# Kernel tuning notes

Hardware: AMD Instinct MI355X
Metric: run time of the kernel (lower is better)

## Reference

```python
import jax, jax.numpy as jnp
import numpy as np

B, S, H, F, E, N, K = 2, 4096, 1024, 3584, 8, 2, 2


def setup_inputs() -> dict:
    key = jax.random.key(0)
    ks = jax.random.split(key, 6)
    scale_h = 1.0 / np.sqrt(H)
    scale_f = 1.0 / np.sqrt(F)
    return {
        "hidden_states": jax.random.normal(ks[0], (B, S, H), dtype=jnp.float32),
        "gate_w": jax.random.normal(ks[1], (E, H), dtype=jnp.float32) * scale_h,
        "gate2_w": jax.random.normal(ks[2], (N, H), dtype=jnp.float32) * scale_h,
        "w1": jax.random.normal(ks[3], (E, F, H), dtype=jnp.float32) * scale_h,
        "w2": jax.random.normal(ks[4], (E, H, F), dtype=jnp.float32) * scale_f,
        "w3": jax.random.normal(ks[5], (E, F, H), dtype=jnp.float32) * scale_h,
    }


def reference(hidden_states, gate_w, gate2_w, w1, w2, w3):
    b, s, h = hidden_states.shape
    x = hidden_states.reshape(-1, h)  # [T, H]

    # Router: real gate + null-expert gate, concatenated
    router_logits = jnp.concatenate([x @ gate_w.T, x @ gate2_w.T], axis=1)  # [T, E+N]
    rw = jax.nn.softmax(router_logits.astype(jnp.float32), axis=1)
    top_w, sel = jax.lax.top_k(rw, K)  # [T, K]

    # Null experts (idx >= E) get their raw weight; real experts are renormalized
    mask = sel < E
    sw = top_w * mask
    denom = sw.sum(axis=-1, keepdims=True)
    denom = jnp.where(denom == 0, 1.0, denom)
    weights = (sw / denom + top_w * (~mask)).astype(x.dtype)  # [T, K]

    # Per-(token, real-expert) combine weight; null experts drop out (one_hot -> 0)
    combine = jnp.einsum("tke,tk->et", jax.nn.one_hot(sel, E, dtype=x.dtype), weights)  # [E, T]

    def body(acc, p):
        w1e, w2e, w3e, cw = p
        hgate = jax.nn.silu(x @ w1e.T) * (x @ w3e.T)  # [T, F]
        return acc + cw[:, None] * (hgate @ w2e.T), None

    out, _ = jax.lax.scan(body, jnp.zeros_like(x), (w1, w2, w3, combine))
    return out.reshape(b, s, h), router_logits
```

## Files before the change

kernel.cpp:

```cpp
#include <hip/hip_runtime.h>
#include <hip/hip_bf16.h>

namespace {

constexpr int T_TOK = 8192;
constexpr int HDIM  = 1024;
constexpr int FDIM  = 3584;
constexpr int CAP_ROWS = 18432;
constexpr int MAXMT = CAP_ROWS / 256;

typedef __bf16 bf16x8 __attribute__((ext_vector_type(8)));
typedef float  f32x4  __attribute__((ext_vector_type(4)));

__device__ inline unsigned short f2bf(float f) {
  union { float f; unsigned u; } a; a.f = f;
  unsigned r = a.u + 0x7fffu + ((a.u >> 16) & 1u);
  return (unsigned short)(r >> 16);
}

typedef const __attribute__((address_space(1))) void* gptr_t;
typedef __attribute__((address_space(3))) void* lptr_t;
__device__ inline void gload_lds16(const void* g, void* l) {
  __builtin_amdgcn_global_load_lds((gptr_t)g, (lptr_t)l, 16, 0, 0);
}

#define MFMA16(a, b, c) __builtin_amdgcn_mfma_f32_16x16x32_bf16(a, b, c, 0, 0, 0)

__global__ __launch_bounds__(256) void k_router(
    const float* __restrict__ x, const float* __restrict__ gw,
    const float* __restrict__ gw2, float* __restrict__ logits_out,
    int* __restrict__ sel, float* __restrict__ wts)
{
  int t = blockIdx.x * 4 + (threadIdx.x >> 6);
  int lane = threadIdx.x & 63;
  if (t >= T_TOK) return;
  const float* xr = x + (size_t)t * HDIM;
  float acc[10];
#pragma unroll
  for (int e = 0; e < 10; ++e) acc[e] = 0.f;
#pragma unroll
  for (int it = 0; it < 4; ++it) {
    int base = it * 256 + lane * 4;
    float4 xv = *reinterpret_cast<const float4*>(xr + base);
#pragma unroll
    for (int e = 0; e < 8; ++e) {
      float4 g = *reinterpret_cast<const float4*>(gw + e * HDIM + base);
      acc[e] += xv.x * g.x + xv.y * g.y + xv.z * g.z + xv.w * g.w;
    }
#pragma unroll
    for (int e = 0; e < 2; ++e) {
      float4 g = *reinterpret_cast<const float4*>(gw2 + e * HDIM + base);
      acc[8 + e] += xv.x * g.x + xv.y * g.y + xv.z * g.z + xv.w * g.w;
    }
  }
#pragma unroll
  for (int e = 0; e < 10; ++e) {
#pragma unroll
    for (int off = 32; off > 0; off >>= 1)
      acc[e] += __shfl_xor(acc[e], off, 64);
  }
  if (lane == 0) {
    float* lo = logits_out + (size_t)t * 10;
#pragma unroll
    for (int e = 0; e < 10; ++e) lo[e] = acc[e];
    float mx = acc[0];
#pragma unroll
    for (int e = 1; e < 10; ++e) mx = fmaxf(mx, acc[e]);
    float p[10], s = 0.f;
#pragma unroll
    for (int e = 0; e < 10; ++e) { p[e] = __expf(acc[e] - mx); s += p[e]; }
    float inv = 1.f / s;
#pragma unroll
    for (int e = 0; e < 10; ++e) p[e] *= inv;
    int i0 = 0;
    for (int e = 1; e < 10; ++e) if (p[e] > p[i0]) i0 = e;
    int i1 = (i0 == 0) ? 1 : 0;
    for (int e = 0; e < 10; ++e) if (e != i0 && p[e] > p[i1]) i1 = e;
    float w0 = p[i0], w1 = p[i1];
    bool r0 = i0 < 8, r1 = i1 < 8;
    float den = (r0 ? w0 : 0.f) + (r1 ? w1 : 0.f);
    if (den == 0.f) den = 1.f;
    sel[t * 2]     = i0; wts[t * 2]     = r0 ? w0 / den : 0.f;
    sel[t * 2 + 1] = i1; wts[t * 2 + 1] = r1 ? w1 / den : 0.f;
  }
}

__global__ __launch_bounds__(256) void k_histseg(
    const int* __restrict__ sel, int* __restrict__ meta)
{
  __shared__ int part[256][8];
  __shared__ int s_tile0[9];
  int tid = threadIdx.x;
  int c[8];
#pragma unroll
  for (int e = 0; e < 8; ++e) c[e] = 0;
  for (int i = 0; i < 64; ++i) {
    int v = sel[i * 256 + tid];
#pragma unroll
    for (int e = 0; e < 8; ++e) c[e] += (v == e);
  }
#pragma unroll
  for (int e = 0; e < 8; ++e) part[tid][e] = c[e];
  __syncthreads();
  for (int s = 128; s >= 1; s >>= 1) {
    if (tid < s) {
#pragma unroll
      for (int e = 0; e < 8; ++e) part[tid][e] += part[tid + s][e];
    }
    __syncthreads();
  }
  if (tid == 0) {
    int off = 0;
    for (int e = 0; e < 8; ++e) {
      int cnt = part[0][e];
      meta[e] = cnt;
      meta[8 + e] = 0;
      meta[16 + e] = off;
      s_tile0[e] = off >> 8;
      off += (cnt + 255) & ~255;
    }
    meta[24] = off;
    meta[25] = off >> 8;
    s_tile0[8] = off >> 8;
  }
  __syncthreads();
  int nt = s_tile0[8];
  if (tid < nt) {
    int e = 0;
    while (s_tile0[e + 1] <= tid) ++e;
    meta[32 + tid] = e;
  }
}

__global__ __launch_bounds__(256) void k_zeropad(
    const int* __restrict__ meta, unsigned short* __restrict__ xg)
{
  int e = blockIdx.x >> 8, r = blockIdx.x & 255;
  int c = meta[e];
  int pad = (c + 255) & ~255;
  if (c + r >= pad) return;
  size_t row = (size_t)meta[16 + e] + c + r;
  reinterpret_cast<ushort4*>(xg + row * HDIM)[threadIdx.x] = ushort4{0, 0, 0, 0};
}

__global__ __launch_bounds__(256) void k_scatter(
    const float* __restrict__ x, const int* __restrict__ sel,
    int* __restrict__ meta, int* __restrict__ pair_row,
    unsigned short* __restrict__ xg)
{
  __shared__ int s_cnt[8];
  __shared__ int s_base[8];
  __shared__ int s_row[256];
  int tid = threadIdx.x;
  int pair0 = blockIdx.x * 256;
  if (tid < 8) s_cnt[tid] = 0;
  __syncthreads();
  int e = sel[pair0 + tid];
  int rank = -1;
  if (e < 8) rank = atomicAdd(&s_cnt[e], 1);
  __syncthreads();
  if (tid < 8) {
    int c = s_cnt[tid];
    s_base[tid] = c > 0 ? atomicAdd(&meta[8 + tid], c) : 0;
  }
  __syncthreads();
  int row = (e < 8) ? meta[16 + e] + s_base[e] + rank : -1;
  pair_row[pair0 + tid] = row;
  s_row[tid] = row;
  __syncthreads();
  int wid = tid >> 6, lane = tid & 63;
  for (int i = wid; i < 256; i += 4) {
    int r = s_row[i];
    if (r < 0) continue;
    const float* xr = x + (size_t)((pair0 + i) >> 1) * HDIM;
    unsigned short* dst = xg + (size_t)r * HDIM;
#pragma unroll
    for (int it = 0; it < 4; ++it) {
      int base = it * 256 + lane * 4;
      float4 v = *reinterpret_cast<const float4*>(xr + base);
      ushort4 o{f2bf(v.x), f2bf(v.y), f2bf(v.z), f2bf(v.w)};
      *reinterpret_cast<ushort4*>(dst + base) = o;
    }
  }
}

__global__ __launch_bounds__(256) void k_conv3(
    const float* __restrict__ s1, const float* __restrict__ s3,
    const float* __restrict__ s2,
    unsigned short* __restrict__ d1, unsigned short* __restrict__ d3,
    unsigned short* __restrict__ d2,
    long long total, long long rl13, long long ss13,
    long long rl2, long long ss2)
{
  long long i = ((long long)blockIdx.x * 256 + threadIdx.x) * 8;
  if (i >= total) return;
  const float* src; unsigned short* dst; long long rowlen, sstride;
  if (blockIdx.y == 0)      { src = s1; dst = d1; rowlen = rl13; sstride = ss13; }
  else if (blockIdx.y == 1) { src = s3; dst = d3; rowlen = rl13; sstride = ss13; }
  else                      { src = s2; dst = d2; rowlen = rl2;  sstride = ss2;  }
  const float* sp;
  if (rowlen == sstride) {
    sp = src + i;
  } else {
    long long r = i / rowlen, c = i - r * rowlen;
    sp = src + r * sstride + c;
  }
  float4 a = reinterpret_cast<const float4*>(sp)[0];
  float4 b = reinterpret_cast<const float4*>(sp)[1];
  ushort4* d = reinterpret_cast<ushort4*>(dst + i);
  d[0] = ushort4{f2bf(a.x), f2bf(a.y), f2bf(a.z), f2bf(a.w)};
  d[1] = ushort4{f2bf(b.x), f2bf(b.y), f2bf(b.z), f2bf(b.w)};
}

__global__ __launch_bounds__(512, 2) void k_gemm1(
    const unsigned short* __restrict__ xg,
    const unsigned short* __restrict__ wc1,
    const unsigned short* __restrict__ wc3,
    unsigned short* __restrict__ hg,
    const int* __restrict__ meta, int Fc)
{
  __shared__ __attribute__((aligned(128))) char lds[131072];

  int mt = blockIdx.y;
  if (mt >= meta[25]) return;
  int e = meta[32 + mt];
  int mrow0 = mt * 256;
  int fl0 = blockIdx.x * 128;

  int tid = threadIdx.x, lane = tid & 63, wid = tid >> 6;
  int lr = lane & 15, lg = lane >> 4;
  int wr = wid >> 2, wc = wid & 3;

  f32x4 acc1[8][2], acc3[8][2];
  const f32x4 zero = {0.f, 0.f, 0.f, 0.f};
#pragma unroll
  for (int m = 0; m < 8; ++m)
#pragma unroll
    for (int n = 0; n < 2; ++n) { acc1[m][n] = zero; acc3[m][n] = zero; }

  int r0 = tid >> 3;
  int csw = ((tid & 7) ^ (r0 & 7)) * 8;
  int dst0 = tid * 16;

  const unsigned short* pa[4];
  const unsigned short* pb1[2];
  const unsigned short* pb3[2];
  {
    const unsigned short* Ab  = xg + (size_t)mrow0 * HDIM;
    const unsigned short* B1b = wc1 + ((size_t)e * Fc + fl0) * HDIM;
    const unsigned short* B3b = wc3 + ((size_t)e * Fc + fl0) * HDIM;
#pragma unroll
    for (int h = 0; h < 2; ++h)
#pragma unroll
      for (int q = 0; q < 2; ++q)
        pa[h * 2 + q] = Ab + (size_t)(h * 128 + q * 64 + r0) * HDIM + csw;
#pragma unroll
    for (int q = 0; q < 2; ++q) {
      pb1[q] = B1b + (size_t)(q * 64 + r0) * HDIM + csw;
      pb3[q] = B3b + (size_t)(q * 64 + r0) * HDIM + csw;
    }
  }

  auto STAGE = [&](int buf) {
    char* b = lds + buf * 65536;
#pragma unroll
    for (int i = 0; i < 4; ++i) {
      gload_lds16(pa[i], b + (i >> 1) * 16384 + (i & 1) * 8192 + dst0);
      pa[i] += 64;
    }
#pragma unroll
    for (int q = 0; q < 2; ++q) {
      gload_lds16(pb1[q], b + 32768 + q * 8192 + dst0);
      pb1[q] += 64;
      gload_lds16(pb3[q], b + 49152 + q * 8192 + dst0);
      pb3[q] += 64;
    }
  };

  const int fxor = (lr & 7) << 4;

  constexpr int NT = HDIM / 64;
  STAGE(0);
#pragma unroll 1
  for (int t = 0; t < NT; ++t) {
    int c = t & 1;
    if (t < NT - 1) {
      STAGE(c ^ 1);
      asm volatile("s_waitcnt vmcnt(8)" ::: "memory");
    } else {
      asm volatile("s_waitcnt vmcnt(0)" ::: "memory");
    }
    asm volatile("s_barrier" ::: "memory");

    const char* bb = lds + c * 65536;
    const char* ab = bb + wr * 16384;
#pragma unroll
    for (int kk = 0; kk < 2; ++kk) {
      int kbyte = (kk * 64 + lg * 16) ^ fxor;
      bf16x8 b1f[2], b3f[2];
#pragma unroll
      for (int n = 0; n < 2; ++n) {
        int off = (wc * 32 + n * 16 + lr) * 128 + kbyte;
        b1f[n] = *reinterpret_cast<const bf16x8*>(bb + 32768 + off);
        b3f[n] = *reinterpret_cast<const bf16x8*>(bb + 49152 + off);
      }
#pragma unroll
      for (int m = 0; m < 8; ++m) {
        bf16x8 af = *reinterpret_cast<const bf16x8*>(ab + (m * 16 + lr) * 128 + kbyte);
#pragma unroll
        for (int n = 0; n < 2; ++n) {
          acc1[m][n] = MFMA16(af, b1f[n], acc1[m][n]);
          acc3[m][n] = MFMA16(af, b3f[n], acc3[m][n]);
        }
      }
    }
    asm volatile("s_barrier" ::: "memory");
  }

#pragma unroll
  for (int m = 0; m < 8; ++m)
#pragma unroll
    for (int n = 0; n < 2; ++n) {
      int gcol = fl0 + wc * 32 + n * 16 + lr;
#pragma unroll
      for (int j = 0; j < 4; ++j) {
        int grow = mrow0 + wr * 128 + m * 16 + lg * 4 + j;
        float s1 = acc1[m][n][j];
        float s3 = acc3[m][n][j];
        float h = s1 / (1.f + __expf(-s1)) * s3;
        hg[(size_t)grow * Fc + gcol] = f2bf(h);
      }
    }
}

__global__ __launch_bounds__(512, 2) void k_gemm2(
    const unsigned short* __restrict__ hg,
    const unsigned short* __restrict__ wc2,
    float* __restrict__ yrows, const int* __restrict__ meta,
    int Fc, int first)
{
  __shared__ __attribute__((aligned(128))) char lds[98304];

  int mt = blockIdx.y;
  if (mt >= meta[25]) return;
  int e = meta[32 + mt];
  int mrow0 = mt * 256;
  int hcol0 = blockIdx.x * 128;

  int tid = threadIdx.x, lane = tid & 63, wid = tid >> 6;
  int lr = lane & 15, lg = lane >> 4;
  int wr = wid >> 2, wc = wid & 3;

  f32x4 acc[8][2];
  const f32x4 zero = {0.f, 0.f, 0.f, 0.f};
#pragma unroll
  for (int m = 0; m < 8; ++m)
#pragma unroll
    for (int n = 0; n < 2; ++n) acc[m][n] = zero;

  int r0 = tid >> 3;
  int csw = ((tid & 7) ^ (r0 & 7)) * 8;
  int dst0 = tid * 16;

  const unsigned short* pa[4];
  const unsigned short* pb[2];
  {
    const unsigned short* Ab = hg + (size_t)mrow0 * Fc;
    const unsigned short* Bb = wc2 + ((size_t)e * HDIM + hcol0) * Fc;
#pragma unroll
    for (int h = 0; h < 2; ++h)
#pragma unroll
      for (int q = 0; q < 2; ++q)
        pa[h * 2 + q] = Ab + (size_t)(h * 128 + q * 64 + r0) * Fc + csw;
#pragma unroll
    for (int q = 0; q < 2; ++q)
      pb[q] = Bb + (size_t)(q * 64 + r0) * Fc + csw;
  }

  auto STAGE = [&](int buf) {
    char* b = lds + buf * 49152;
#pragma unroll
    for (int i = 0; i < 4; ++i) {
      gload_lds16(pa[i], b + (i >> 1) * 16384 + (i & 1) * 8192 + dst0);
      pa[i] += 64;
    }
#pragma unroll
    for (int q = 0; q < 2; ++q) {
      gload_lds16(pb[q], b + 32768 + q * 8192 + dst0);
      pb[q] += 64;
    }
  };

  const int fxor = (lr & 7) << 4;

  int NT = Fc / 64;
  STAGE(0);
#pragma unroll 1
  for (int t = 0; t < NT; ++t) {
    int c = t & 1;
    if (t < NT - 1) {
      STAGE(c ^ 1);
      asm volatile("s_waitcnt vmcnt(6)" ::: "memory");
    } else {
      asm volatile("s_waitcnt vmcnt(0)" ::: "memory");
    }
    asm volatile("s_barrier" ::: "memory");

    const char* bb = lds + c * 49152;
    const char* ab = bb + wr * 16384;
#pragma unroll
    for (int kk = 0; kk < 2; ++kk) {
      int kbyte = (kk * 64 + lg * 16) ^ fxor;
      bf16x8 bf[2];
#pragma unroll
      for (int n = 0; n < 2; ++n) {
        int off = (wc * 32 + n * 16 + lr) * 128 + kbyte;
        bf[n] = *reinterpret_cast<const bf16x8*>(bb + 32768 + off);
      }
#pragma unroll
      for (int m = 0; m < 8; ++m) {
        bf16x8 af = *reinterpret_cast<const bf16x8*>(ab + (m * 16 + lr) * 128 + kbyte);
#pragma unroll
        for (int n = 0; n < 2; ++n)
          acc[m][n] = MFMA16(af, bf[n], acc[m][n]);
      }
    }
    asm volatile("s_barrier" ::: "memory");
  }

#pragma unroll
  for (int m = 0; m < 8; ++m)
#pragma unroll
    for (int n = 0; n < 2; ++n) {
      int gcol = hcol0 + wc * 32 + n * 16 + lr;
#pragma unroll
      for (int j = 0; j < 4; ++j) {
        int grow = mrow0 + wr * 128 + m * 16 + lg * 4 + j;
        float* yp = yrows + (size_t)grow * HDIM + gcol;
        float v = acc[m][n][j];
        if (first) *yp = v; else *yp += v;
      }
    }
}

__global__ __launch_bounds__(256) void k_combine(
    const float* __restrict__ yrows, const int* __restrict__ pair_row,
    const float* __restrict__ wts, float* __restrict__ out)
{
  int t = blockIdx.x * 4 + (threadIdx.x >> 6);
  int lane = threadIdx.x & 63;
  if (t >= T_TOK) return;
  int r0 = pair_row[t * 2], r1 = pair_row[t * 2 + 1];
  float w0 = (r0 >= 0) ? wts[t * 2] : 0.f;
  float w1 = (r1 >= 0) ? wts[t * 2 + 1] : 0.f;
  const float* y0 = yrows + (size_t)(r0 >= 0 ? r0 : 0) * HDIM;
  const float* y1 = yrows + (size_t)(r1 >= 0 ? r1 : 0) * HDIM;
  float* op = out + (size_t)t * HDIM;
#pragma unroll
  for (int it = 0; it < 4; ++it) {
    int base = it * 256 + lane * 4;
    float4 a = *reinterpret_cast<const float4*>(y0 + base);
    float4 b = *reinterpret_cast<const float4*>(y1 + base);
    float4 r{w0 * a.x + w1 * b.x, w0 * a.y + w1 * b.y,
             w0 * a.z + w1 * b.z, w0 * a.w + w1 * b.w};
    *reinterpret_cast<float4*>(op + base) = r;
  }
}

}

extern "C" void kernel_launch(void* const* d_in, const int* in_sizes, int n_in,
                              void* d_out, int out_size, void* d_ws, size_t ws_size,
                              hipStream_t stream)
{
  const float* x   = (const float*)d_in[0];
  const float* gw  = (const float*)d_in[1];
  const float* gw2 = (const float*)d_in[2];
  const float* w1  = (const float*)d_in[3];
  const float* w2  = (const float*)d_in[4];
  const float* w3  = (const float*)d_in[5];
  float* out = (float*)d_out;
  float* logits_out = out + (size_t)T_TOK * HDIM;

  char* p = (char*)d_ws;
  int* meta = (int*)p;            p += 1024;
  int* sel = (int*)p;             p += T_TOK * 2 * sizeof(int);
  float* wts = (float*)p;         p += T_TOK * 2 * sizeof(float);
  int* pair_row = (int*)p;        p += T_TOK * 2 * sizeof(int);
  unsigned short* xg = (unsigned short*)p;  p += (size_t)CAP_ROWS * HDIM * 2;
  float* yrows = (float*)p;                 p += (size_t)CAP_ROWS * HDIM * 4;
  size_t fixed = (size_t)(p - (char*)d_ws);

  int nf = 28;
  const int opts[6] = {1, 2, 4, 7, 14, 28};
  for (int i = 0; i < 6; ++i) {
    size_t Fc_i = FDIM / opts[i];
    size_t need = fixed + 3 * 16384 * Fc_i + (size_t)CAP_ROWS * Fc_i * 2;
    if (need <= ws_size) { nf = opts[i]; break; }
  }
  int Fc = FDIM / nf;

  unsigned short* wc1 = (unsigned short*)p;  p += (size_t)16384 * Fc;
  unsigned short* wc3 = (unsigned short*)p;  p += (size_t)16384 * Fc;
  unsigned short* wc2 = (unsigned short*)p;  p += (size_t)16384 * Fc;
  unsigned short* hg  = (unsigned short*)p;

  k_router<<<T_TOK / 4, 256, 0, stream>>>(x, gw, gw2, logits_out, sel, wts);
  k_histseg<<<1, 256, 0, stream>>>(sel, meta);
  k_zeropad<<<2048, 256, 0, stream>>>(meta, xg);
  k_scatter<<<T_TOK * 2 / 256, 256, 0, stream>>>(x, sel, meta, pair_row, xg);

  long long total = 8LL * Fc * HDIM;
  int ncb = (int)(total / 8 / 256);
  for (int c = 0; c < nf; ++c) {
    long long c0 = (long long)c * Fc;
    k_conv3<<<dim3(ncb, 3), 256, 0, stream>>>(
        w1 + c0 * HDIM, w3 + c0 * HDIM, w2 + c0, wc1, wc3, wc2,
        total, (long long)Fc * HDIM, (long long)FDIM * HDIM,
        (long long)Fc, (long long)FDIM);

    k_gemm1<<<dim3(Fc / 128, MAXMT), 512, 0, stream>>>(xg, wc1, wc3, hg, meta, Fc);
    k_gemm2<<<dim3(HDIM / 128, MAXMT), 512, 0, stream>>>(hg, wc2, yrows, meta, Fc, c == 0 ? 1 : 0);
  }
  k_combine<<<T_TOK / 4, 256, 0, stream>>>(yrows, pair_row, wts, out);
}
```

Measured before the change: 530.0 us.

## Split GEMM K-steps into four phases interleaving staged loads with prioritized MFMA

```diff
diff --git a/kernel.cpp b/kernel.cpp
--- a/kernel.cpp
+++ b/kernel.cpp
@@ -25,6 +25,15 @@
 }
 
 #define MFMA16(a, b, c) __builtin_amdgcn_mfma_f32_16x16x32_bf16(a, b, c, 0, 0, 0)
+
+#define BAR()      asm volatile("s_barrier" ::: "memory")
+#define VMC(N)     asm volatile("s_waitcnt vmcnt(" #N ")" ::: "memory")
+#define SYNC_PRE() do { BAR(); \
+  asm volatile("s_waitcnt lgkmcnt(0)" ::: "memory"); \
+  __builtin_amdgcn_sched_barrier(0); \
+  __builtin_amdgcn_s_setprio(1); } while (0)
+#define SYNC_POST() do { __builtin_amdgcn_s_setprio(0); \
+  __builtin_amdgcn_sched_barrier(0); } while (0)
 
 __global__ __launch_bounds__(256) void k_router(
     const float* __restrict__ x, const float* __restrict__ gw,
@@ -230,6 +239,7 @@
   int tid = threadIdx.x, lane = tid & 63, wid = tid >> 6;
   int lr = lane & 15, lg = lane >> 4;
   int wr = wid >> 2, wc = wid & 3;
+  const int fxor = (lr & 7) << 4;
 
   f32x4 acc1[8][2], acc3[8][2];
   const f32x4 zero = {0.f, 0.f, 0.f, 0.f};
@@ -238,13 +248,12 @@
 #pragma unroll
     for (int n = 0; n < 2; ++n) { acc1[m][n] = zero; acc3[m][n] = zero; }
 
-  int r0 = tid >> 3;
-  int csw = ((tid & 7) ^ (r0 & 7)) * 8;
+  int srow = tid >> 3;
+  int csw = ((tid & 7) ^ (srow & 7)) * 8;
   int dst0 = tid * 16;
 
-  const unsigned short* pa[4];
-  const unsigned short* pb1[2];
-  const unsigned short* pb3[2];
+  const unsigned short* pA[2][2];
+  const unsigned short* pB[2][2];
   {
     const unsigned short* Ab  = xg + (size_t)mrow0 * HDIM;
     const unsigned short* B1b = wc1 + ((size_t)e * Fc + fl0) * HDIM;
@@ -252,69 +261,81 @@
 #pragma unroll
     for (int h = 0; h < 2; ++h)
 #pragma unroll
-      for (int q = 0; q < 2; ++q)
-        pa[h * 2 + q] = Ab + (size_t)(h * 128 + q * 64 + r0) * HDIM + csw;
-#pragma unroll
-    for (int q = 0; q < 2; ++q) {
-      pb1[q] = B1b + (size_t)(q * 64 + r0) * HDIM + csw;
-      pb3[q] = B3b + (size_t)(q * 64 + r0) * HDIM + csw;
-    }
-  }
-
-  auto STAGE = [&](int buf) {
-    char* b = lds + buf * 65536;
-#pragma unroll
-    for (int i = 0; i < 4; ++i) {
-      gload_lds16(pa[i], b + (i >> 1) * 16384 + (i & 1) * 8192 + dst0);
-      pa[i] += 64;
-    }
-#pragma unroll
-    for (int q = 0; q < 2; ++q) {
-      gload_lds16(pb1[q], b + 32768 + q * 8192 + dst0);
-      pb1[q] += 64;
-      gload_lds16(pb3[q], b + 49152 + q * 8192 + dst0);
-      pb3[q] += 64;
-    }
-  };
-
-  const int fxor = (lr & 7) << 4;
+      for (int mh = 0; mh < 2; ++mh)
+        pA[h][mh] = Ab + (size_t)(h * 128 + mh * 64 + srow) * HDIM + csw;
+    int bcol = (srow >> 4) * 32 + (srow & 15);
+#pragma unroll
+    for (int n = 0; n < 2; ++n) {
+      pB[0][n] = B1b + (size_t)(bcol + n * 16) * HDIM + csw;
+      pB[1][n] = B3b + (size_t)(bcol + n * 16) * HDIM + csw;
+    }
+  }
+
+#define G1_STAGE_A(BUF, MH) do { \
+  char* b_ = lds + (BUF) * 65536; \
+  gload_lds16(pA[0][MH], b_ + ((0) * 2 + (MH)) * 8192 + dst0); pA[0][MH] += 64; \
+  gload_lds16(pA[1][MH], b_ + ((1) * 2 + (MH)) * 8192 + dst0); pA[1][MH] += 64; \
+} while (0)
+#define G1_STAGE_B(BUF, N) do { \
+  char* b_ = lds + (BUF) * 65536; \
+  gload_lds16(pB[0][N], b_ + 32768 + 0 * 16384 + (N) * 8192 + dst0); pB[0][N] += 64; \
+  gload_lds16(pB[1][N], b_ + 32768 + 1 * 16384 + (N) * 8192 + dst0); pB[1][N] += 64; \
+} while (0)
+
+#define G1_READ_A(MH) do { \
+  const char* qb_ = bb + (wr * 2 + (MH)) * 8192; \
+  _Pragma("unroll") for (int kk = 0; kk < 2; ++kk) { \
+    int kb_ = (kk * 64 + lg * 16) ^ fxor; \
+    _Pragma("unroll") for (int i = 0; i < 4; ++i) \
+      aH[kk][i] = *reinterpret_cast<const bf16x8*>(qb_ + (i * 16 + lr) * 128 + kb_); \
+  } } while (0)
+#define G1_READ_B(N) do { \
+  int rr_ = (wc * 16 + lr) * 128; \
+  _Pragma("unroll") for (int kk = 0; kk < 2; ++kk) { \
+    int kb_ = (kk * 64 + lg * 16) ^ fxor; \
+    b1f[kk] = *reinterpret_cast<const bf16x8*>(bb + 32768 + (N) * 8192 + rr_ + kb_); \
+    b3f[kk] = *reinterpret_cast<const bf16x8*>(bb + 49152 + (N) * 8192 + rr_ + kb_); \
+  } } while (0)
+#define G1_MFMA(MH, N) do { \
+  _Pragma("unroll") for (int kk = 0; kk < 2; ++kk) \
+    _Pragma("unroll") for (int i = 0; i < 4; ++i) { \
+      acc1[(MH) * 4 + i][N] = MFMA16(aH[kk][i], b1f[kk], acc1[(MH) * 4 + i][N]); \
+      acc3[(MH) * 4 + i][N] = MFMA16(aH[kk][i], b3f[kk], acc3[(MH) * 4 + i][N]); \
+    } } while (0)
 
   constexpr int NT = HDIM / 64;
-  STAGE(0);
+  G1_STAGE_A(0, 0); G1_STAGE_B(0, 0); G1_STAGE_B(0, 1); G1_STAGE_A(0, 1);
+  VMC(4); BAR();
+
 #pragma unroll 1
   for (int t = 0; t < NT; ++t) {
-    int c = t & 1;
-    if (t < NT - 1) {
-      STAGE(c ^ 1);
-      asm volatile("s_waitcnt vmcnt(8)" ::: "memory");
-    } else {
-      asm volatile("s_waitcnt vmcnt(0)" ::: "memory");
-    }
-    asm volatile("s_barrier" ::: "memory");
-
+    int c = t & 1, nb = c ^ 1;
+    bool st = (t < NT - 1);
     const char* bb = lds + c * 65536;
-    const char* ab = bb + wr * 16384;
-#pragma unroll
-    for (int kk = 0; kk < 2; ++kk) {
-      int kbyte = (kk * 64 + lg * 16) ^ fxor;
-      bf16x8 b1f[2], b3f[2];
-#pragma unroll
-      for (int n = 0; n < 2; ++n) {
-        int off = (wc * 32 + n * 16 + lr) * 128 + kbyte;
-        b1f[n] = *reinterpret_cast<const bf16x8*>(bb + 32768 + off);
-        b3f[n] = *reinterpret_cast<const bf16x8*>(bb + 49152 + off);
-      }
-#pragma unroll
-      for (int m = 0; m < 8; ++m) {
-        bf16x8 af = *reinterpret_cast<const bf16x8*>(ab + (m * 16 + lr) * 128 + kbyte);
-#pragma unroll
-        for (int n = 0; n < 2; ++n) {
-          acc1[m][n] = MFMA16(af, b1f[n], acc1[m][n]);
-          acc3[m][n] = MFMA16(af, b3f[n], acc3[m][n]);
-        }
-      }
-    }
-    asm volatile("s_barrier" ::: "memory");
+    bf16x8 aH[2][4], b1f[2], b3f[2];
+
+    G1_READ_A(0); G1_READ_B(0);
+    if (st) G1_STAGE_A(nb, 0);
+    SYNC_PRE(); G1_MFMA(0, 0); SYNC_POST();
+    if (st) { VMC(4); } else { VMC(2); }
+    BAR();
+
+    G1_READ_B(1);
+    if (st) G1_STAGE_B(nb, 0);
+    SYNC_PRE(); G1_MFMA(0, 1); SYNC_POST();
+    if (st) { VMC(4); } else { VMC(0); }
+    BAR();
+
+    G1_READ_A(1); G1_READ_B(0);
+    if (st) G1_STAGE_B(nb, 1);
+    SYNC_PRE(); G1_MFMA(1, 0); SYNC_POST();
+    BAR();
+
+    G1_READ_B(1);
+    if (st) G1_STAGE_A(nb, 1);
+    SYNC_PRE(); G1_MFMA(1, 1); SYNC_POST();
+    if (st) { VMC(4); }
+    BAR();
   }
 
 #pragma unroll
@@ -350,6 +371,7 @@
   int tid = threadIdx.x, lane = tid & 63, wid = tid >> 6;
   int lr = lane & 15, lg = lane >> 4;
   int wr = wid >> 2, wc = wid & 3;
+  const int fxor = (lr & 7) << 4;
 
   f32x4 acc[8][2];
   const f32x4 zero = {0.f, 0.f, 0.f, 0.f};
@@ -358,74 +380,87 @@
 #pragma unroll
     for (int n = 0; n < 2; ++n) acc[m][n] = zero;
 
-  int r0 = tid >> 3;
-  int csw = ((tid & 7) ^ (r0 & 7)) * 8;
+  int srow = tid >> 3;
+  int csw = ((tid & 7) ^ (srow & 7)) * 8;
   int dst0 = tid * 16;
 
-  const unsigned short* pa[4];
-  const unsigned short* pb[2];
+  const unsigned short* pA[2][2];
+  const unsigned short* pB[2];
   {
     const unsigned short* Ab = hg + (size_t)mrow0 * Fc;
     const unsigned short* Bb = wc2 + ((size_t)e * HDIM + hcol0) * Fc;
 #pragma unroll
     for (int h = 0; h < 2; ++h)
 #pragma unroll
-      for (int q = 0; q < 2; ++q)
-        pa[h * 2 + q] = Ab + (size_t)(h * 128 + q * 64 + r0) * Fc + csw;
-#pragma unroll
-    for (int q = 0; q < 2; ++q)
-      pb[q] = Bb + (size_t)(q * 64 + r0) * Fc + csw;
-  }
-
-  auto STAGE = [&](int buf) {
-    char* b = lds + buf * 49152;
-#pragma unroll
-    for (int i = 0; i < 4; ++i) {
-      gload_lds16(pa[i], b + (i >> 1) * 16384 + (i & 1) * 8192 + dst0);
-      pa[i] += 64;
-    }
-#pragma unroll
-    for (int q = 0; q < 2; ++q) {
-      gload_lds16(pb[q], b + 32768 + q * 8192 + dst0);
-      pb[q] += 64;
-    }
-  };
-
-  const int fxor = (lr & 7) << 4;
+      for (int mh = 0; mh < 2; ++mh)
+        pA[h][mh] = Ab + (size_t)(h * 128 + mh * 64 + srow) * Fc + csw;
+    int bcol = (srow >> 4) * 32 + (srow & 15);
+#pragma unroll
+    for (int n = 0; n < 2; ++n)
+      pB[n] = Bb + (size_t)(bcol + n * 16) * Fc + csw;
+  }
+
+#define G2_STAGE_A(BUF, MH) do { \
+  char* b_ = lds + (BUF) * 49152; \
+  gload_lds16(pA[0][MH], b_ + ((0) * 2 + (MH)) * 8192 + dst0); pA[0][MH] += 64; \
+  gload_lds16(pA[1][MH], b_ + ((1) * 2 + (MH)) * 8192 + dst0); pA[1][MH] += 64; \
+} while (0)
+#define G2_STAGE_B(BUF, N) do { \
+  char* b_ = lds + (BUF) * 49152; \
+  gload_lds16(pB[N], b_ + 32768 + (N) * 8192 + dst0); pB[N] += 64; \
+} while (0)
+#define G2_READ_A(MH) do { \
+  const char* qb_ = bb + (wr * 2 + (MH)) * 8192; \
+  _Pragma("unroll") for (int kk = 0; kk < 2; ++kk) { \
+    int kb_ = (kk * 64 + lg * 16) ^ fxor; \
+    _Pragma("unroll") for (int i = 0; i < 4; ++i) \
+      aH[kk][i] = *reinterpret_cast<const bf16x8*>(qb_ + (i * 16 + lr) * 128 + kb_); \
+  } } while (0)
+#define G2_READ_B(N) do { \
+  int rr_ = (wc * 16 + lr) * 128; \
+  _Pragma("unroll") for (int kk = 0; kk < 2; ++kk) { \
+    int kb_ = (kk * 64 + lg * 16) ^ fxor; \
+    bf[kk] = *reinterpret_cast<const bf16x8*>(bb + 32768 + (N) * 8192 + rr_ + kb_); \
+  } } while (0)
+#define G2_MFMA(MH, N) do { \
+  _Pragma("unroll") for (int kk = 0; kk < 2; ++kk) \
+    _Pragma("unroll") for (int i = 0; i < 4; ++i) \
+      acc[(MH) * 4 + i][N] = MFMA16(aH[kk][i], bf[kk], acc[(MH) * 4 + i][N]); \
+  } while (0)
 
   int NT = Fc / 64;
-  STAGE(0);
+  G2_STAGE_A(0, 0); G2_STAGE_B(0, 0); G2_STAGE_B(0, 1); G2_STAGE_A(0, 1);
+  VMC(3); BAR();
+
 #pragma unroll 1
   for (int t = 0; t < NT; ++t) {
-    int c = t & 1;
-    if (t < NT - 1) {
-      STAGE(c ^ 1);
-      asm volatile("s_waitcnt vmcnt(6)" ::: "memory");
-    } else {
-      asm volatile("s_waitcnt vmcnt(0)" ::: "memory");
-    }
-    asm volatile("s_barrier" ::: "memory");
-
+    int c = t & 1, nb = c ^ 1;
+    bool st = (t < NT - 1);
     const char* bb = lds + c * 49152;
-    const char* ab = bb + wr * 16384;
-#pragma unroll
-    for (int kk = 0; kk < 2; ++kk) {
-      int kbyte = (kk * 64 + lg * 16) ^ fxor;
-      bf16x8 bf[2];
-#pragma unroll
-      for (int n = 0; n < 2; ++n) {
-        int off = (wc * 32 + n * 16 + lr) * 128 + kbyte;
-        bf[n] = *reinterpret_cast<const bf16x8*>(bb + 32768 + off);
-      }
-#pragma unroll
-      for (int m = 0; m < 8; ++m) {
-        bf16x8 af = *reinterpret_cast<const bf16x8*>(ab + (m * 16 + lr) * 128 + kbyte);
-#pragma unroll
-        for (int n = 0; n < 2; ++n)
-          acc[m][n] = MFMA16(af, bf[n], acc[m][n]);
-      }
-    }
-    asm volatile("s_barrier" ::: "memory");
+    bf16x8 aH[2][4], bf[2];
+
+    G2_READ_A(0); G2_READ_B(0);
+    if (st) G2_STAGE_A(nb, 0);
+    SYNC_PRE(); G2_MFMA(0, 0); SYNC_POST();
+    if (st) { VMC(4); } else { VMC(2); }
+    BAR();
+
+    G2_READ_B(1);
+    if (st) G2_STAGE_B(nb, 0);
+    SYNC_PRE(); G2_MFMA(0, 1); SYNC_POST();
+    if (st) { VMC(3); } else { VMC(0); }
+    BAR();
+
+    G2_READ_A(1); G2_READ_B(0);
+    if (st) G2_STAGE_B(nb, 1);
+    SYNC_PRE(); G2_MFMA(1, 0); SYNC_POST();
+    BAR();
+
+    G2_READ_B(1);
+    if (st) G2_STAGE_A(nb, 1);
+    SYNC_PRE(); G2_MFMA(1, 1); SYNC_POST();
+    if (st) { VMC(3); }
+    BAR();
   }
 
 #pragma unroll
```

Measured after the change: 543.0 us. 2.4% more time.
